# Kernel optimization log

Hardware: AMD Instinct MI355X
Metric: run time of the kernel (lower is better)

## Reference

```python
import jax, jax.numpy as jnp
import numpy as np
from jax import lax

BLOCK_SIZE = 5
GAMMA = 0.02


def setup_inputs() -> dict:
    key = jax.random.key(0)
    kx, km = jax.random.split(key)
    N, C, H, W = 64, 64, 80, 80
    x = jax.random.normal(kx, (N, C, H, W), dtype=jnp.float32)
    # Bernoulli(gamma) sample, materialized as an int32 0/1 mask (the module's
    # internal randomness, fixed for deterministic reference comparison).
    mask = (jax.random.uniform(km, (N, C, H, W)) < GAMMA).astype(jnp.int32)
    return {"x": x, "mask": mask}


def _dropblock(x, mask, block_size):
    m = mask.astype(x.dtype)  # 0/1 seed mask, shape (N,C,H,W)
    # Original scatters each seed (h,w) into [h, h+bs) x [w, w+bs) (clipped at
    # H,W). Equivalent dense form: block_mask[i,j] = max over m[i-dh, j-dw],
    # dh,dw in [0,bs) -> sliding-window max with top/left padding of bs-1.
    if block_size > 1:
        block_mask = lax.reduce_window(
            m,
            jnp.array(0.0, x.dtype),
            lax.max,
            window_dimensions=(1, 1, block_size, block_size),
            window_strides=(1, 1, 1, 1),
            padding=((0, 0), (0, 0), (block_size - 1, 0), (block_size - 1, 0)),
        )
    else:
        block_mask = m
    inv_blk_mask = 1.0 - block_mask
    countM = jnp.array(m.size, x.dtype)
    count_ones = inv_blk_mask.sum()
    return inv_blk_mask * x * (countM / count_ones)


def reference(x, mask):
    return _dropblock(x, mask, BLOCK_SIZE)
```

## Files before the change

### kernel.cpp

```cpp
#include <hip/hip_runtime.h>

#define DB_H 80
#define DB_W 80
#define DB_PLANE (DB_H * DB_W)
#define DB_NPLANES 4096
#define DB_ROW_WORDS 3
#define DB_PLANE_WORDS (DB_H * DB_ROW_WORDS)
#define DB_TOTAL (DB_PLANE * DB_NPLANES)
#define DB_COUNT_F 26214400.0f
#define DB_CNT_BYTES (DB_NPLANES * 4)
#define PPBLK 2
#define WPB 4

__global__ __launch_bounds__(256) void db_mask_kernel(
    const int* __restrict__ mask,
    unsigned int* __restrict__ bits,
    unsigned int* __restrict__ counts)
{
    __shared__ unsigned long long P[PPBLK][104];
    __shared__ unsigned int RO[PPBLK][DB_PLANE_WORDS];
    __shared__ unsigned int ZP[PPBLK][2];
    const int t = threadIdx.x;
    const int wid = t >> 6, lane = t & 63;
    const int pib = wid >> 1, half = wid & 1;
    const int plane = blockIdx.x * PPBLK + pib;
    const int* mp = mask + plane * DB_PLANE;
    unsigned long long* Pp = P[pib];
    unsigned int* ro = RO[pib];

    {
        const int base0 = half * 50;
        int v[10], w[10];
        #pragma unroll
        for (int k = 0; k < 10; ++k) v[k] = mp[(base0 + k) * 64 + lane];
        #pragma unroll 1
        for (int c = 0; c < 5; ++c) {
            const int base = base0 + c * 10;
            if (c < 4) {
                #pragma unroll
                for (int k = 0; k < 10; ++k)
                    w[k] = mp[(base + 10 + k) * 64 + lane];
            }
            #pragma unroll
            for (int k = 0; k < 10; ++k) {
                unsigned long long bal = __ballot(v[k] & 1);
                if (lane == 0) Pp[base + k] = bal;
            }
            #pragma unroll
            for (int k = 0; k < 10; ++k) v[k] = w[k];
        }
    }
    if (t < 2 * 4) P[t >> 2][100 + (t & 3)] = 0ULL;
    __syncthreads();

    if (lane < 40) {
        const int r = half * 40 + lane;
        const int bitpos = r * DB_W;
        const int q = bitpos >> 6, off = bitpos & 63;
        unsigned long long a, b;
        if (off) {
            a = (Pp[q] >> off) | (Pp[q + 1] << (64 - off));
            b = (Pp[q + 1] >> off) | (Pp[q + 2] << (64 - off));
        } else {
            a = Pp[q]; b = Pp[q + 1];
        }
        b &= 0xFFFFULL;
        unsigned long long ra = a, rb = b;
        #pragma unroll
        for (int s = 1; s <= 4; ++s) {
            ra |= a << s;
            rb |= (b << s) | (a >> (64 - s));
        }
        rb &= 0xFFFFULL;
        ro[r * 3 + 0] = (unsigned int)ra;
        ro[r * 3 + 1] = (unsigned int)(ra >> 32);
        ro[r * 3 + 2] = (unsigned int)rb;
    }
    __syncthreads();

    unsigned int zeros = 0;
    if (lane < 40) {
        const int i = half * 40 + lane;
        const int lo = (i >= 4) ? i - 4 : 0;
        unsigned int c0 = 0, c1 = 0, c2 = 0;
        for (int ii = lo; ii <= i; ++ii) {
            c0 |= ro[ii * 3 + 0];
            c1 |= ro[ii * 3 + 1];
            c2 |= ro[ii * 3 + 2];
        }
        zeros = 80u - __popc(c0) - __popc(c1) - __popc(c2);
        unsigned int* bp = bits + plane * DB_PLANE_WORDS + i * 3;
        bp[0] = c0; bp[1] = c1; bp[2] = c2;
    }
    for (int off = 32; off > 0; off >>= 1)
        zeros += (unsigned int)__shfl_down((int)zeros, off, 64);
    if (lane == 0) ZP[pib][half] = zeros;
    __syncthreads();
    if (lane == 0 && half == 0)
        counts[plane] = ZP[pib][0] + ZP[pib][1];
}

__global__ __launch_bounds__(256) void db_apply_bits(
    const float4* __restrict__ x,
    const unsigned int* __restrict__ bits,
    const unsigned int* __restrict__ counts,
    float4* __restrict__ out)
{
    __shared__ float s_scale;
    __shared__ unsigned int s_part[4];
    {
        const uint4* cp = (const uint4*)counts;
        unsigned int c = 0;
        #pragma unroll
        for (int k = 0; k < 4; ++k) {
            uint4 v = cp[k * 256 + threadIdx.x];
            c += v.x + v.y + v.z + v.w;
        }
        for (int off = 32; off > 0; off >>= 1)
            c += (unsigned int)__shfl_down((int)c, off, 64);
        if ((threadIdx.x & 63) == 0) s_part[threadIdx.x >> 6] = c;
        __syncthreads();
        if (threadIdx.x == 0)
            s_scale = DB_COUNT_F /
                      (float)(s_part[0] + s_part[1] + s_part[2] + s_part[3]);
        __syncthreads();
    }
    const float scale = s_scale;
    const int NG = DB_TOTAL / 4;
    const int stride = gridDim.x * blockDim.x;
    #pragma unroll 2
    for (int g = blockIdx.x * blockDim.x + threadIdx.x; g < NG; g += stride) {
        int e = g * 4;
        int plane = e / DB_PLANE;
        int ep = e - plane * DB_PLANE;
        int i = ep / DB_W;
        int j = ep - i * DB_W;
        unsigned int nib =
            (bits[plane * DB_PLANE_WORDS + i * 3 + (j >> 5)] >> (j & 31)) & 0xFu;
        float4 v = make_float4(0.f, 0.f, 0.f, 0.f);
        if (nib != 0xFu) v = x[g];
        float4 o;
        o.x = (nib & 1u) ? 0.0f : v.x * scale;
        o.y = (nib & 2u) ? 0.0f : v.y * scale;
        o.z = (nib & 4u) ? 0.0f : v.z * scale;
        o.w = (nib & 8u) ? 0.0f : v.w * scale;
        out[g] = o;
    }
}

__global__ __launch_bounds__(256) void db_count_kernel(
    const int* __restrict__ mask,
    unsigned int* __restrict__ counts)
{
    __shared__ unsigned long long P[WPB][104];
    __shared__ unsigned int RO[WPB][DB_PLANE_WORDS];
    const int wid = threadIdx.x >> 6, lane = threadIdx.x & 63;
    const int plane = blockIdx.x * WPB + wid;
    const int* mp = mask + plane * DB_PLANE;
    unsigned long long* Pp = P[wid];
    unsigned int* ro = RO[wid];
    #pragma unroll 1
    for (int c = 0; c < 10; ++c) {
        int v[10];
        #pragma unroll
        for (int k = 0; k < 10; ++k) v[k] = mp[(c * 10 + k) * 64 + lane];
        #pragma unroll
        for (int k = 0; k < 10; ++k) {
            unsigned long long bal = __ballot(v[k] & 1);
            if (lane == 0) Pp[c * 10 + k] = bal;
        }
    }
    if (lane < 4) Pp[100 + lane] = 0ULL;
    __syncthreads();
    for (int r = lane; r < DB_H; r += 64) {
        const int bitpos = r * DB_W;
        const int q = bitpos >> 6, off = bitpos & 63;
        unsigned long long a, b;
        if (off) {
            a = (Pp[q] >> off) | (Pp[q + 1] << (64 - off));
            b = (Pp[q + 1] >> off) | (Pp[q + 2] << (64 - off));
        } else {
            a = Pp[q]; b = Pp[q + 1];
        }
        b &= 0xFFFFULL;
        unsigned long long ra = a, rb = b;
        #pragma unroll
        for (int s = 1; s <= 4; ++s) {
            ra |= a << s;
            rb |= (b << s) | (a >> (64 - s));
        }
        rb &= 0xFFFFULL;
        ro[r * 3 + 0] = (unsigned int)ra;
        ro[r * 3 + 1] = (unsigned int)(ra >> 32);
        ro[r * 3 + 2] = (unsigned int)rb;
    }
    __syncthreads();
    unsigned int zeros = 0;
    for (int i = lane; i < DB_H; i += 64) {
        const int lo = (i >= 4) ? i - 4 : 0;
        unsigned int c0 = 0, c1 = 0, c2 = 0;
        for (int ii = lo; ii <= i; ++ii) {
            c0 |= ro[ii * 3 + 0];
            c1 |= ro[ii * 3 + 1];
            c2 |= ro[ii * 3 + 2];
        }
        zeros += 80u - __popc(c0) - __popc(c1) - __popc(c2);
    }
    for (int off = 32; off > 0; off >>= 1)
        zeros += (unsigned int)__shfl_down((int)zeros, off, 64);
    if (lane == 0) counts[plane] = zeros;
}

__global__ __launch_bounds__(256) void db_apply_recompute(
    const float* __restrict__ x,
    const int* __restrict__ mask,
    const unsigned int* __restrict__ counts,
    float* __restrict__ out)
{
    __shared__ unsigned long long P[WPB][104];
    __shared__ unsigned int RO[WPB][DB_PLANE_WORDS];
    __shared__ unsigned int BM[WPB][DB_PLANE_WORDS];
    __shared__ float s_scale;
    __shared__ unsigned int s_part[4];
    {
        const uint4* cp = (const uint4*)counts;
        unsigned int c = 0;
        #pragma unroll
        for (int k = 0; k < 4; ++k) {
            uint4 v = cp[k * 256 + threadIdx.x];
            c += v.x + v.y + v.z + v.w;
        }
        for (int off = 32; off > 0; off >>= 1)
            c += (unsigned int)__shfl_down((int)c, off, 64);
        if ((threadIdx.x & 63) == 0) s_part[threadIdx.x >> 6] = c;
        __syncthreads();
        if (threadIdx.x == 0)
            s_scale = DB_COUNT_F /
                      (float)(s_part[0] + s_part[1] + s_part[2] + s_part[3]);
        __syncthreads();
    }
    const float scale = s_scale;
    const int wid = threadIdx.x >> 6, lane = threadIdx.x & 63;
    const int plane = blockIdx.x * WPB + wid;
    const int* mp = mask + plane * DB_PLANE;
    unsigned long long* Pp = P[wid];
    unsigned int* ro = RO[wid];
    #pragma unroll 1
    for (int c = 0; c < 10; ++c) {
        int v[10];
        #pragma unroll
        for (int k = 0; k < 10; ++k) v[k] = mp[(c * 10 + k) * 64 + lane];
        #pragma unroll
        for (int k = 0; k < 10; ++k) {
            unsigned long long bal = __ballot(v[k] & 1);
            if (lane == 0) Pp[c * 10 + k] = bal;
        }
    }
    if (lane < 4) Pp[100 + lane] = 0ULL;
    __syncthreads();
    for (int r = lane; r < DB_H; r += 64) {
        const int bitpos = r * DB_W;
        const int q = bitpos >> 6, off = bitpos & 63;
        unsigned long long a, b;
        if (off) {
            a = (Pp[q] >> off) | (Pp[q + 1] << (64 - off));
            b = (Pp[q + 1] >> off) | (Pp[q + 2] << (64 - off));
        } else {
            a = Pp[q]; b = Pp[q + 1];
        }
        b &= 0xFFFFULL;
        unsigned long long ra = a, rb = b;
        #pragma unroll
        for (int s = 1; s <= 4; ++s) {
            ra |= a << s;
            rb |= (b << s) | (a >> (64 - s));
        }
        rb &= 0xFFFFULL;
        ro[r * 3 + 0] = (unsigned int)ra;
        ro[r * 3 + 1] = (unsigned int)(ra >> 32);
        ro[r * 3 + 2] = (unsigned int)rb;
    }
    __syncthreads();
    unsigned int* bmp = BM[wid];
    for (int i = lane; i < DB_H; i += 64) {
        const int lo = (i >= 4) ? i - 4 : 0;
        unsigned int c0 = 0, c1 = 0, c2 = 0;
        for (int ii = lo; ii <= i; ++ii) {
            c0 |= ro[ii * 3 + 0];
            c1 |= ro[ii * 3 + 1];
            c2 |= ro[ii * 3 + 2];
        }
        bmp[i * 3 + 0] = c0; bmp[i * 3 + 1] = c1; bmp[i * 3 + 2] = c2;
    }
    __syncthreads();
    const float* xp = x + plane * DB_PLANE;
    float* op = out + plane * DB_PLANE;
    for (int e = lane; e < DB_PLANE; e += 64) {
        int i = e / DB_W, j = e - i * DB_W;
        unsigned int wb = bmp[i * 3 + (j >> 5)] >> (j & 31);
        op[e] = (wb & 1u) ? 0.0f : xp[e] * scale;
    }
}

extern "C" void kernel_launch(void* const* d_in, const int* in_sizes, int n_in,
                              void* d_out, int out_size, void* d_ws, size_t ws_size,
                              hipStream_t stream) {
    const float* x = (const float*)d_in[0];
    const int* mask = (const int*)d_in[1];
    float* out = (float*)d_out;

    unsigned int* counts = (unsigned int*)d_ws;
    unsigned int* bits = (unsigned int*)((char*)d_ws + DB_CNT_BYTES);
    const size_t bits_bytes = (size_t)DB_NPLANES * DB_PLANE_WORDS * 4;
    const bool use_bits = ws_size >= DB_CNT_BYTES + bits_bytes;

    if (use_bits) {
        db_mask_kernel<<<DB_NPLANES / PPBLK, 256, 0, stream>>>(mask, bits,
                                                               counts);
        db_apply_bits<<<2048, 256, 0, stream>>>(
            (const float4*)x, bits, counts, (float4*)out);
    } else {
        db_count_kernel<<<DB_NPLANES / WPB, 256, 0, stream>>>(mask, counts);
        db_apply_recompute<<<DB_NPLANES / WPB, 256, 0, stream>>>(
            x, mask, counts, out);
    }
}
```

Measured before the change: 65.35 us.

## Process mask planes per wavefront without block barriers and pipeline loads across planes

The mask kernel now gives each wavefront whole planes (two per wave, eight per block) instead of splitting a plane across two waves. This drops every __syncthreads and the shared partial-count exchange, and the prefetch of the next chunk of 10 rows runs continuously across plane boundaries. The trade-offs are fewer blocks (512 instead of 2048), less parallelism inside each plane, and per-wave serial row loops over 80 rows with 64 lanes, which leaves some lanes idle.

After: 69.04 us. 5.6% more time.

```diff
diff --git a/kernel.cpp b/kernel.cpp
--- a/kernel.cpp
+++ b/kernel.cpp
@@ -9,7 +9,8 @@
 #define DB_TOTAL (DB_PLANE * DB_NPLANES)
 #define DB_COUNT_F 26214400.0f
 #define DB_CNT_BYTES (DB_NPLANES * 4)
-#define PPBLK 2
+#define PPW 2
+#define MASK_BLOCKS (DB_NPLANES / (4 * PPW))
 #define WPB 4
 
 __global__ __launch_bounds__(256) void db_mask_kernel(
@@ -17,87 +18,91 @@
     unsigned int* __restrict__ bits,
     unsigned int* __restrict__ counts)
 {
-    __shared__ unsigned long long P[PPBLK][104];
-    __shared__ unsigned int RO[PPBLK][DB_PLANE_WORDS];
-    __shared__ unsigned int ZP[PPBLK][2];
-    const int t = threadIdx.x;
-    const int wid = t >> 6, lane = t & 63;
-    const int pib = wid >> 1, half = wid & 1;
-    const int plane = blockIdx.x * PPBLK + pib;
-    const int* mp = mask + plane * DB_PLANE;
-    unsigned long long* Pp = P[pib];
-    unsigned int* ro = RO[pib];
-
+    __shared__ unsigned long long P[4][104];
+    __shared__ unsigned int RO[4][DB_PLANE_WORDS];
+    const int wid = threadIdx.x >> 6, lane = threadIdx.x & 63;
+    const int plane0 = (blockIdx.x * 4 + wid) * PPW;
+    unsigned long long* Pp = P[wid];
+    unsigned int* ro = RO[wid];
+
+    int v[10], w[10];
     {
-        const int base0 = half * 50;
-        int v[10], w[10];
-        #pragma unroll
-        for (int k = 0; k < 10; ++k) v[k] = mp[(base0 + k) * 64 + lane];
+        const int* mp0 = mask + (size_t)plane0 * DB_PLANE;
+        #pragma unroll
+        for (int k = 0; k < 10; ++k) v[k] = mp0[k * 64 + lane];
+        #pragma unroll
+        for (int k = 0; k < 10; ++k) w[k] = mp0[(10 + k) * 64 + lane];
+    }
+
+    #pragma unroll 1
+    for (int p = 0; p < PPW; ++p) {
         #pragma unroll 1
-        for (int c = 0; c < 5; ++c) {
-            const int base = base0 + c * 10;
-            if (c < 4) {
+        for (int c = 0; c < 10; ++c) {
+            const int b2 = p * 10 + c + 2;
+            int u[10];
+            if (b2 < 10 * PPW) {
+                const int np = b2 / 10, nc = b2 - np * 10;
+                const int* mpn = mask + (size_t)(plane0 + np) * DB_PLANE;
                 #pragma unroll
                 for (int k = 0; k < 10; ++k)
-                    w[k] = mp[(base + 10 + k) * 64 + lane];
+                    u[k] = mpn[(nc * 10 + k) * 64 + lane];
+            } else {
+                #pragma unroll
+                for (int k = 0; k < 10; ++k) u[k] = 0;
             }
             #pragma unroll
             for (int k = 0; k < 10; ++k) {
                 unsigned long long bal = __ballot(v[k] & 1);
-                if (lane == 0) Pp[base + k] = bal;
+                if (lane == 0) Pp[c * 10 + k] = bal;
             }
             #pragma unroll
-            for (int k = 0; k < 10; ++k) v[k] = w[k];
-        }
-    }
-    if (t < 2 * 4) P[t >> 2][100 + (t & 3)] = 0ULL;
-    __syncthreads();
-
-    if (lane < 40) {
-        const int r = half * 40 + lane;
-        const int bitpos = r * DB_W;
-        const int q = bitpos >> 6, off = bitpos & 63;
-        unsigned long long a, b;
-        if (off) {
-            a = (Pp[q] >> off) | (Pp[q + 1] << (64 - off));
-            b = (Pp[q + 1] >> off) | (Pp[q + 2] << (64 - off));
-        } else {
-            a = Pp[q]; b = Pp[q + 1];
-        }
-        b &= 0xFFFFULL;
-        unsigned long long ra = a, rb = b;
-        #pragma unroll
-        for (int s = 1; s <= 4; ++s) {
-            ra |= a << s;
-            rb |= (b << s) | (a >> (64 - s));
-        }
-        rb &= 0xFFFFULL;
-        ro[r * 3 + 0] = (unsigned int)ra;
-        ro[r * 3 + 1] = (unsigned int)(ra >> 32);
-        ro[r * 3 + 2] = (unsigned int)rb;
-    }
-    __syncthreads();
-
-    unsigned int zeros = 0;
-    if (lane < 40) {
-        const int i = half * 40 + lane;
-        const int lo = (i >= 4) ? i - 4 : 0;
-        unsigned int c0 = 0, c1 = 0, c2 = 0;
-        for (int ii = lo; ii <= i; ++ii) {
-            c0 |= ro[ii * 3 + 0];
-            c1 |= ro[ii * 3 + 1];
-            c2 |= ro[ii * 3 + 2];
-        }
-        zeros = 80u - __popc(c0) - __popc(c1) - __popc(c2);
-        unsigned int* bp = bits + plane * DB_PLANE_WORDS + i * 3;
-        bp[0] = c0; bp[1] = c1; bp[2] = c2;
-    }
-    for (int off = 32; off > 0; off >>= 1)
-        zeros += (unsigned int)__shfl_down((int)zeros, off, 64);
-    if (lane == 0) ZP[pib][half] = zeros;
-    __syncthreads();
-    if (lane == 0 && half == 0)
-        counts[plane] = ZP[pib][0] + ZP[pib][1];
+            for (int k = 0; k < 10; ++k) { v[k] = w[k]; w[k] = u[k]; }
+        }
+        if (lane < 4) Pp[100 + lane] = 0ULL;
+
+        #pragma unroll 1
+        for (int r = lane; r < DB_H; r += 64) {
+            const int bitpos = r * DB_W;
+            const int q = bitpos >> 6, off = bitpos & 63;
+            unsigned long long a, b;
+            if (off) {
+                a = (Pp[q] >> off) | (Pp[q + 1] << (64 - off));
+                b = (Pp[q + 1] >> off) | (Pp[q + 2] << (64 - off));
+            } else {
+                a = Pp[q]; b = Pp[q + 1];
+            }
+            b &= 0xFFFFULL;
+            unsigned long long ra = a, rb = b;
+            #pragma unroll
+            for (int s = 1; s <= 4; ++s) {
+                ra |= a << s;
+                rb |= (b << s) | (a >> (64 - s));
+            }
+            rb &= 0xFFFFULL;
+            ro[r * 3 + 0] = (unsigned int)ra;
+            ro[r * 3 + 1] = (unsigned int)(ra >> 32);
+            ro[r * 3 + 2] = (unsigned int)rb;
+        }
+
+        unsigned int zeros = 0;
+        #pragma unroll 1
+        for (int i = lane; i < DB_H; i += 64) {
+            const int lo = (i >= 4) ? i - 4 : 0;
+            unsigned int c0 = 0, c1 = 0, c2 = 0;
+            for (int ii = lo; ii <= i; ++ii) {
+                c0 |= ro[ii * 3 + 0];
+                c1 |= ro[ii * 3 + 1];
+                c2 |= ro[ii * 3 + 2];
+            }
+            zeros += 80u - __popc(c0) - __popc(c1) - __popc(c2);
+            unsigned int* bp =
+                bits + (size_t)(plane0 + p) * DB_PLANE_WORDS + i * 3;
+            bp[0] = c0; bp[1] = c1; bp[2] = c2;
+        }
+        for (int off = 32; off > 0; off >>= 1)
+            zeros += (unsigned int)__shfl_down((int)zeros, off, 64);
+        if (lane == 0) counts[plane0 + p] = zeros;
+    }
 }
 
 __global__ __launch_bounds__(256) void db_apply_bits(
@@ -315,8 +320,7 @@
     const bool use_bits = ws_size >= DB_CNT_BYTES + bits_bytes;
 
     if (use_bits) {
-        db_mask_kernel<<<DB_NPLANES / PPBLK, 256, 0, stream>>>(mask, bits,
-                                                               counts);
+        db_mask_kernel<<<MASK_BLOCKS, 256, 0, stream>>>(mask, bits, counts);
         db_apply_bits<<<2048, 256, 0, stream>>>(
             (const float4*)x, bits, counts, (float4*)out);
     } else {
```
